# Kernel optimization log

Hardware: AMD Instinct MI355X
Metric: run time of the kernel (lower is better)

## Reference

```python
import jax, jax.numpy as jnp
import numpy as np

D_MODEL = 1024
D_HIDDEN = 16384
N_TOKENS = 8192
K = 32


def setup_inputs() -> dict:
    key = jax.random.key(0)
    k1, k2, k3 = jax.random.split(key, 3)
    x = jax.random.normal(k1, (N_TOKENS, D_MODEL), dtype=jnp.float32)
    # encoder.weight: [d_hidden, d_model] (torch Linear convention)
    W_enc = jax.random.normal(k2, (D_HIDDEN, D_MODEL), dtype=jnp.float32) * (1.0 / np.sqrt(D_MODEL))
    # decoder.weight: [d_model, d_hidden], column-normalized as in __init__
    W_dec = jax.random.normal(k3, (D_MODEL, D_HIDDEN), dtype=jnp.float32)
    W_dec = W_dec / (jnp.linalg.norm(W_dec, axis=0, keepdims=True) + 1e-8)
    b_pre = jnp.zeros((D_MODEL,), dtype=jnp.float32)
    b_act = jnp.zeros((D_HIDDEN,), dtype=jnp.float32)
    return {"x": x, "W_enc": W_enc, "W_dec": W_dec, "b_pre": b_pre, "b_act": b_act, "k": K}


def reference(x, W_enc, W_dec, b_pre, b_act, k):
    # encode
    x_cent = x - b_pre                                   # [N, d_model]
    pre_acts = jnp.einsum('nd,hd->nh', x_cent, W_enc) + b_act  # [N, d_hidden]
    # top-k hard activation with straight-through estimator
    vals, inds = jax.lax.top_k(pre_acts, k)              # [N, k]
    rows = jnp.arange(pre_acts.shape[0])[:, None]        # [N, 1]
    hard = jnp.zeros_like(pre_acts).at[rows, inds].set(jax.nn.relu(vals))
    sparse_acts = hard + (pre_acts - jax.lax.stop_gradient(pre_acts))
    # decode
    recon = jnp.einsum('nh,dh->nd', sparse_acts, W_dec) + b_pre  # [N, d_model]
    return (recon, sparse_acts, pre_acts)
```

## Files before the change

### kernel.cpp

```cpp
#include <hip/hip_runtime.h>
#include <hip/hip_bf16.h>

#define N_TOK   8192
#define DM      1024
#define DH      16384
#define KTOP    32
#define NCAND   256
#define DZ      0.08f
#define NT      16

typedef unsigned int uint;
typedef __attribute__((ext_vector_type(8))) short bf16x8;
typedef __attribute__((ext_vector_type(4))) float f32x4;

__device__ inline ushort f2bf(float f) {
    uint u = __float_as_uint(f);
    uint r = (u + 0x7FFFu + ((u >> 16) & 1u)) >> 16;
    return (ushort)r;
}
__device__ inline float bf2f(ushort u) {
    return __uint_as_float(((uint)u) << 16);
}

__device__ inline void load_lds16(const void* g, void* l) {
    __builtin_amdgcn_global_load_lds(
        (const __attribute__((address_space(1))) void*)g,
        (__attribute__((address_space(3))) void*)l, 16, 0, 0);
}

__global__ __launch_bounds__(256) void conv_x(
    const float* __restrict__ x, const float* __restrict__ b_pre,
    ushort* __restrict__ A)
{
    int i = (blockIdx.x * 256 + threadIdx.x) * 4;
    float4 v = *(const float4*)&x[i];
    float4 b = *(const float4*)&b_pre[i & (DM - 1)];
    ushort4 o;
    o.x = f2bf(v.x - b.x); o.y = f2bf(v.y - b.y);
    o.z = f2bf(v.z - b.z); o.w = f2bf(v.w - b.w);
    *(ushort4*)&A[i] = o;
}

__global__ __launch_bounds__(256) void conv_w(
    const float* __restrict__ W, ushort* __restrict__ B)
{
    int i = (blockIdx.x * 256 + threadIdx.x) * 4;
    float4 v = *(const float4*)&W[i];
    ushort4 o;
    o.x = f2bf(v.x); o.y = f2bf(v.y); o.z = f2bf(v.z); o.w = f2bf(v.w);
    *(ushort4*)&B[i] = o;
}

#define LDS_A(par, ks)  ((par) * 65536 + (ks) * 16384)
#define LDS_B(par, ks)  ((par) * 65536 + 32768 + (ks) * 16384)

__global__ __launch_bounds__(512, 2) void gemm8ph(
    const ushort* __restrict__ A, const ushort* __restrict__ B,
    const float* __restrict__ b_act, float* __restrict__ pre)
{
    __shared__ __align__(16) char smem[131072];

    const int tid  = threadIdx.x;
    const int wid  = tid >> 6;
    const int lane = tid & 63;
    const int wm   = wid >> 2;
    const int wn   = wid & 3;

    const int swz  = (blockIdx.x & 7) * 256 + (blockIdx.x >> 3);
    const int row0 = (swz & 31) * 256;
    const int col0 = (swz >> 5) * 256;

    f32x4 acc[8][4] = {};

    auto stage = [&](const ushort* __restrict__ g, int grow0, int gk0,
                     int region) {
        #pragma unroll
        for (int i = 0; i < 2; ++i) {
            int c    = i * 512 + wid * 64 + lane;
            int row  = c >> 2;
            int slot = (c & 3) ^ ((row >> 1) & 3);
            load_lds16(g + (size_t)(grow0 + row) * DM + gk0 + slot * 8,
                       smem + region + (i * 512 + wid * 64) * 16);
        }
    };
    auto ld_frag = [&](int region, int row) -> bf16x8 {
        int slot = (lane >> 4) ^ ((row >> 1) & 3);
        return *(const bf16x8*)(smem + region + row * 64 + slot * 16);
    };

    stage(A, row0, 0,  LDS_A(0, 0));
    stage(B, col0, 0,  LDS_B(0, 0));
    stage(A, row0, 32, LDS_A(0, 1));
    stage(B, col0, 32, LDS_B(0, 1));

    for (int t = 0; t < NT; ++t) {
        const int par  = t & 1;
        const int npar = par ^ 1;
        const int tn   = (t < NT - 1) ? t + 1 : t;
        const int k0n  = tn * 64;
        const int ar   = wm * 128 + (lane & 15);
        const int br   = wn * 64 + (lane & 15);

        stage(A, row0, k0n, LDS_A(npar, 0));
        asm volatile("s_waitcnt vmcnt(6)" ::: "memory");
        __builtin_amdgcn_s_barrier();
        asm volatile("" ::: "memory");

        bf16x8 af[8];
        #pragma unroll
        for (int mf = 0; mf < 8; ++mf)
            af[mf] = ld_frag(LDS_A(par, 0), ar + mf * 16);
        {
            bf16x8 b0 = ld_frag(LDS_B(par, 0), br);
            bf16x8 b1 = ld_frag(LDS_B(par, 0), br + 16);
            __builtin_amdgcn_s_setprio(1);
            #pragma unroll
            for (int mf = 0; mf < 8; ++mf) {
                acc[mf][0] = __builtin_amdgcn_mfma_f32_16x16x32_bf16(af[mf], b0, acc[mf][0], 0, 0, 0);
                acc[mf][1] = __builtin_amdgcn_mfma_f32_16x16x32_bf16(af[mf], b1, acc[mf][1], 0, 0, 0);
            }
            __builtin_amdgcn_s_setprio(0);
        }

        stage(B, col0, k0n, LDS_B(npar, 0));
        {
            bf16x8 b2 = ld_frag(LDS_B(par, 0), br + 32);
            bf16x8 b3 = ld_frag(LDS_B(par, 0), br + 48);
            __builtin_amdgcn_s_setprio(1);
            #pragma unroll
            for (int mf = 0; mf < 8; ++mf) {
                acc[mf][2] = __builtin_amdgcn_mfma_f32_16x16x32_bf16(af[mf], b2, acc[mf][2], 0, 0, 0);
                acc[mf][3] = __builtin_amdgcn_mfma_f32_16x16x32_bf16(af[mf], b3, acc[mf][3], 0, 0, 0);
            }
            __builtin_amdgcn_s_setprio(0);
        }

        stage(A, row0, k0n + 32, LDS_A(npar, 1));
        asm volatile("s_waitcnt vmcnt(6)" ::: "memory");
        __builtin_amdgcn_s_barrier();
        asm volatile("" ::: "memory");

        #pragma unroll
        for (int mf = 0; mf < 8; ++mf)
            af[mf] = ld_frag(LDS_A(par, 1), ar + mf * 16);
        {
            bf16x8 b0 = ld_frag(LDS_B(par, 1), br);
            bf16x8 b1 = ld_frag(LDS_B(par, 1), br + 16);
            __builtin_amdgcn_s_setprio(1);
            #pragma unroll
            for (int mf = 0; mf < 8; ++mf) {
                acc[mf][0] = __builtin_amdgcn_mfma_f32_16x16x32_bf16(af[mf], b0, acc[mf][0], 0, 0, 0);
                acc[mf][1] = __builtin_amdgcn_mfma_f32_16x16x32_bf16(af[mf], b1, acc[mf][1], 0, 0, 0);
            }
            __builtin_amdgcn_s_setprio(0);
        }

        stage(B, col0, k0n + 32, LDS_B(npar, 1));
        {
            bf16x8 b2 = ld_frag(LDS_B(par, 1), br + 32);
            bf16x8 b3 = ld_frag(LDS_B(par, 1), br + 48);
            __builtin_amdgcn_s_setprio(1);
            #pragma unroll
            for (int mf = 0; mf < 8; ++mf) {
                acc[mf][2] = __builtin_amdgcn_mfma_f32_16x16x32_bf16(af[mf], b2, acc[mf][2], 0, 0, 0);
                acc[mf][3] = __builtin_amdgcn_mfma_f32_16x16x32_bf16(af[mf], b3, acc[mf][3], 0, 0, 0);
            }
            __builtin_amdgcn_s_setprio(0);
        }
    }

    float bav[4];
    #pragma unroll
    for (int nf = 0; nf < 4; ++nf)
        bav[nf] = b_act[col0 + wn * 64 + nf * 16 + (lane & 15)];
    #pragma unroll
    for (int mf = 0; mf < 8; ++mf) {
        const int grow = row0 + wm * 128 + mf * 16 + (lane >> 4) * 4;
        const int gcol = col0 + wn * 64 + (lane & 15);
        #pragma unroll
        for (int r = 0; r < 4; ++r) {
            #pragma unroll
            for (int nf = 0; nf < 4; ++nf)
                pre[(size_t)(grow + r) * DH + gcol + nf * 16] = acc[mf][nf][r] + bav[nf];
        }
    }
}

__global__ __launch_bounds__(512) void topk_cand(
    const float* __restrict__ pre, float* __restrict__ sparse,
    float* __restrict__ cval, int* __restrict__ cidx, int* __restrict__ ccnt)
{
    const int row = blockIdx.x;
    const int tid = threadIdx.x;
    const float* __restrict__ p = pre + (size_t)row * DH;

    float v[32];
    #pragma unroll
    for (int j = 0; j < 32; ++j) v[j] = p[j * 512 + tid];

    float4 z = {0.f, 0.f, 0.f, 0.f};
    float4* srow = (float4*)(sparse + (size_t)row * DH);
    #pragma unroll
    for (int i = 0; i < 8; ++i) srow[tid + i * 512] = z;

    __shared__ int scount;
    float lo = -30.f, hi = 30.f, t = 0.f;
    for (int it = 0; it < 20; ++it) {
        t = 0.5f * (lo + hi);
        int c = 0;
        #pragma unroll
        for (int j = 0; j < 32; ++j) c += (v[j] > t);
        #pragma unroll
        for (int off = 32; off; off >>= 1) c += __shfl_down(c, off);
        if (tid == 0) scount = 0;
        __syncthreads();
        if ((tid & 63) == 0) atomicAdd(&scount, c);
        __syncthreads();
        int total = scount;
        __syncthreads();
        if (total >= 96 && total <= 250) break;
        if (total < 96) hi = t; else lo = t;
    }

    __shared__ int wpos;
    __shared__ float scv[NCAND];
    __shared__ int   sci[NCAND];
    if (tid == 0) wpos = 0;
    __syncthreads();
    #pragma unroll
    for (int j = 0; j < 32; ++j) {
        if (v[j] > t) {
            int pz = atomicAdd(&wpos, 1);
            if (pz < NCAND) { scv[pz] = v[j]; sci[pz] = j * 512 + tid; }
        }
    }
    __syncthreads();
    int n = min(wpos, NCAND);
    if (tid == 0) ccnt[row] = n;
    if (tid < NCAND) {
        cval[(size_t)row * NCAND + tid] = (tid < n) ? scv[tid] : -1e30f;
        cidx[(size_t)row * NCAND + tid] = (tid < n) ? sci[tid] : -1;
    }
}

__global__ __launch_bounds__(256) void fix_topk(
    const float* __restrict__ x, const float* __restrict__ b_pre,
    const float* __restrict__ W, const float* __restrict__ b_act,
    const float* __restrict__ cval, const int* __restrict__ cidx,
    float* __restrict__ sparse, float* __restrict__ vals, int* __restrict__ inds)
{
    const int row = blockIdx.x;
    const int tid = threadIdx.x;
    const int wid = tid >> 6, lane = tid & 63;

    __shared__ float xs[DM];
    for (int i = tid; i < DM; i += 256)
        xs[i] = x[(size_t)row * DM + i] - b_pre[i];

    __shared__ float sv[NCAND];
    __shared__ float sex[NCAND];
    __shared__ int   si[NCAND];
    __shared__ int   zlist[NCAND];
    __shared__ unsigned char zf[NCAND];
    __shared__ float sa32;
    __shared__ int   scin, zn;

    const float v  = cval[(size_t)row * NCAND + tid];
    const int   id = cidx[(size_t)row * NCAND + tid];
    sv[tid] = v; si[tid] = id; sex[tid] = v;
    if (tid == 0) { scin = 0; zn = 0; }
    if (tid < KTOP) {
        vals[(size_t)row * KTOP + tid] = 0.f;
        inds[(size_t)row * KTOP + tid] = -1;
    }
    __syncthreads();

    int rank = 0;
    for (int j = 0; j < NCAND; ++j) {
        float ov = sv[j];
        rank += (ov > v) || (ov == v && si[j] < id);
    }
    if (rank == 31) sa32 = v;
    __syncthreads();

    const float a32 = sa32;
    const bool cin  = v > a32 + DZ;
    const bool zone = !cin && (v >= a32 - DZ) && (id >= 0);

    unsigned long long bal = __ballot(cin);
    if (lane == 0) atomicAdd(&scin, (int)__popcll(bal));
    if (zone) { int p = atomicAdd(&zn, 1); zlist[p] = tid; }
    zf[tid] = zone ? 1 : 0;
    __syncthreads();

    const int cin_total = scin;
    const int znum = zn;

    for (int m = wid; m < znum; m += 4) {
        int t = zlist[m];
        int h = si[t];
        const float* wrow = W + (size_t)h * DM;
        float s = 0.f;
        #pragma unroll
        for (int c = 0; c < 16; ++c)
            s = fmaf(xs[lane + c * 64], wrow[lane + c * 64], s);
        #pragma unroll
        for (int off = 32; off; off >>= 1) s += __shfl_down(s, off);
        if (lane == 0) sex[t] = s + b_act[h];
    }
    __syncthreads();

    int slot = -1;
    float outv = 0.f;
    if (cin) { slot = rank; outv = v; }
    else if (zone) {
        float ev = sex[tid];
        int zrank = 0;
        for (int j = 0; j < NCAND; ++j) {
            if (zf[j]) {
                float ov = sex[j];
                zrank += (ov > ev) || (ov == ev && si[j] < id);
            }
        }
        if (zrank < KTOP - cin_total) { slot = cin_total + zrank; outv = ev; }
    }
    if (slot >= 0) {
        float r = fmaxf(outv, 0.f);
        vals[(size_t)row * KTOP + slot] = r;
        inds[(size_t)row * KTOP + slot] = id;
        sparse[(size_t)row * DH + id] = r;
    }
}

__global__ __launch_bounds__(256) void transpose_dec(
    const float* __restrict__ W, ushort* __restrict__ WT)
{
    __shared__ float t[32][33];
    const int tx = threadIdx.x;
    const int ty = threadIdx.y;
    const int h0 = blockIdx.x * 32;
    const int d0 = blockIdx.y * 32;
    #pragma unroll
    for (int r = 0; r < 4; ++r)
        t[ty + r * 8][tx] = W[(size_t)(d0 + ty + r * 8) * DH + h0 + tx];
    __syncthreads();
    #pragma unroll
    for (int r = 0; r < 4; ++r)
        WT[(size_t)(h0 + ty + r * 8) * DM + d0 + tx] = f2bf(t[tx][ty + r * 8]);
}

__global__ __launch_bounds__(256) void recon_kernel(
    const float* __restrict__ vals, const int* __restrict__ inds,
    const ushort* __restrict__ wdecT, const float* __restrict__ b_pre,
    float* __restrict__ recon)
{
    const int row = blockIdx.x;
    const int tid = threadIdx.x;
    __shared__ float lval[KTOP];
    __shared__ int   lind[KTOP];
    if (tid < KTOP) {
        lval[tid] = vals[(size_t)row * KTOP + tid];
        lind[tid] = inds[(size_t)row * KTOP + tid];
    }
    __syncthreads();

    const int d = tid * 4;
    float4 a = *(const float4*)&b_pre[d];
    #pragma unroll 8
    for (int j = 0; j < KTOP; ++j) {
        float vj = lval[j];
        int h = lind[j];
        if (vj != 0.f && h >= 0) {
            ushort4 w = *(const ushort4*)&wdecT[(size_t)h * DM + d];
            a.x = fmaf(vj, bf2f(w.x), a.x);
            a.y = fmaf(vj, bf2f(w.y), a.y);
            a.z = fmaf(vj, bf2f(w.z), a.z);
            a.w = fmaf(vj, bf2f(w.w), a.w);
        }
    }
    *(float4*)&recon[(size_t)row * DM + d] = a;
}

extern "C" void kernel_launch(void* const* d_in, const int* in_sizes, int n_in,
                              void* d_out, int out_size, void* d_ws, size_t ws_size,
                              hipStream_t stream)
{
    const float* x     = (const float*)d_in[0];
    const float* W_enc = (const float*)d_in[1];
    const float* W_dec = (const float*)d_in[2];
    const float* b_pre = (const float*)d_in[3];
    const float* b_act = (const float*)d_in[4];

    float* recon  = (float*)d_out;
    float* sparse = recon + (size_t)N_TOK * DM;
    float* pre    = sparse + (size_t)N_TOK * DH;

    ushort* Abf = (ushort*)sparse;
    ushort* Bbf = Abf + (size_t)N_TOK * DM;

    float*  cval  = (float*)d_ws;
    int*    cidx  = (int*)(cval + (size_t)N_TOK * NCAND);
    int*    ccnt  = cidx + (size_t)N_TOK * NCAND;
    float*  vals  = (float*)(ccnt + N_TOK);
    int*    inds  = (int*)(vals + (size_t)N_TOK * KTOP);
    ushort* wdecT = (ushort*)(inds + (size_t)N_TOK * KTOP);

    conv_x<<<N_TOK * DM / 1024, 256, 0, stream>>>(x, b_pre, Abf);
    conv_w<<<DH * DM / 1024, 256, 0, stream>>>(W_enc, Bbf);

    gemm8ph<<<(N_TOK / 256) * (DH / 256), 512, 0, stream>>>(Abf, Bbf, b_act, pre);

    transpose_dec<<<dim3(DH / 32, DM / 32), dim3(32, 8), 0, stream>>>(W_dec, wdecT);

    topk_cand<<<N_TOK, 512, 0, stream>>>(pre, sparse, cval, cidx, ccnt);

    fix_topk<<<N_TOK, 256, 0, stream>>>(x, b_pre, W_enc, b_act,
                                        cval, cidx, sparse, vals, inds);

    recon_kernel<<<N_TOK, 256, 0, stream>>>(vals, inds, wdecT, b_pre, recon);
}
```

Measured before the change: 929.0 us.

## Collect top-k candidates in GEMM epilogue and fuse candidate selection into fix kernel

The GEMM epilogue now thresholds each pre-activation against a fixed cutoff and records up to 8 packed bf16 value/index candidates per row per column tile into a workspace, flagging any overflow. A single fused top-k kernel reads these compact candidates instead of re-reading the full 16384-wide pre-activation row, and falls back to the old bisection search only for flagged or out-of-range rows. This removes a full pass over the large pre-activation matrix and one kernel launch. The cost is shared-memory atomics in the GEMM epilogue, a memset of the candidate buffer, and a data-dependent fixed threshold tuned to the input distribution. The last K-step is also peeled out of the GEMM loop so it no longer issues a redundant prefetch.

```diff
diff --git a/kernel.cpp b/kernel.cpp
--- a/kernel.cpp
+++ b/kernel.cpp
@@ -5,7 +5,9 @@
 #define DM      1024
 #define DH      16384
 #define KTOP    32
-#define NCAND   256
+#define NCAND   512
+#define SLOTS   8
+#define CAND_T  2.2f
 #define DZ      0.08f
 #define NT      16
 
@@ -56,7 +58,8 @@
 
 __global__ __launch_bounds__(512, 2) void gemm8ph(
     const ushort* __restrict__ A, const ushort* __restrict__ B,
-    const float* __restrict__ b_act, float* __restrict__ pre)
+    const float* __restrict__ b_act, float* __restrict__ pre,
+    uint* __restrict__ cand, uint* __restrict__ flags)
 {
     __shared__ __align__(16) char smem[131072];
 
@@ -88,18 +91,18 @@
         return *(const bf16x8*)(smem + region + row * 64 + slot * 16);
     };
 
+    const int ar = wm * 128 + (lane & 15);
+    const int br = wn * 64 + (lane & 15);
+
     stage(A, row0, 0,  LDS_A(0, 0));
     stage(B, col0, 0,  LDS_B(0, 0));
     stage(A, row0, 32, LDS_A(0, 1));
     stage(B, col0, 32, LDS_B(0, 1));
 
-    for (int t = 0; t < NT; ++t) {
+    for (int t = 0; t < NT - 1; ++t) {
         const int par  = t & 1;
         const int npar = par ^ 1;
-        const int tn   = (t < NT - 1) ? t + 1 : t;
-        const int k0n  = tn * 64;
-        const int ar   = wm * 128 + (lane & 15);
-        const int br   = wn * 64 + (lane & 15);
+        const int k0n  = (t + 1) * 64;
 
         stage(A, row0, k0n, LDS_A(npar, 0));
         asm volatile("s_waitcnt vmcnt(6)" ::: "memory");
@@ -121,7 +124,6 @@
             }
             __builtin_amdgcn_s_setprio(0);
         }
-
         stage(B, col0, k0n, LDS_B(npar, 0));
         {
             bf16x8 b2 = ld_frag(LDS_B(par, 0), br + 32);
@@ -134,7 +136,6 @@
             }
             __builtin_amdgcn_s_setprio(0);
         }
-
         stage(A, row0, k0n + 32, LDS_A(npar, 1));
         asm volatile("s_waitcnt vmcnt(6)" ::: "memory");
         __builtin_amdgcn_s_barrier();
@@ -154,7 +155,6 @@
             }
             __builtin_amdgcn_s_setprio(0);
         }
-
         stage(B, col0, k0n + 32, LDS_B(npar, 1));
         {
             bf16x8 b2 = ld_frag(LDS_B(par, 1), br + 32);
@@ -168,93 +168,115 @@
             __builtin_amdgcn_s_setprio(0);
         }
     }
+
+    {
+        const int par = (NT - 1) & 1;
+        asm volatile("s_waitcnt vmcnt(4)" ::: "memory");
+        __builtin_amdgcn_s_barrier();
+        asm volatile("" ::: "memory");
+
+        bf16x8 af[8];
+        #pragma unroll
+        for (int mf = 0; mf < 8; ++mf)
+            af[mf] = ld_frag(LDS_A(par, 0), ar + mf * 16);
+        {
+            bf16x8 b0 = ld_frag(LDS_B(par, 0), br);
+            bf16x8 b1 = ld_frag(LDS_B(par, 0), br + 16);
+            bf16x8 b2 = ld_frag(LDS_B(par, 0), br + 32);
+            bf16x8 b3 = ld_frag(LDS_B(par, 0), br + 48);
+            __builtin_amdgcn_s_setprio(1);
+            #pragma unroll
+            for (int mf = 0; mf < 8; ++mf) {
+                acc[mf][0] = __builtin_amdgcn_mfma_f32_16x16x32_bf16(af[mf], b0, acc[mf][0], 0, 0, 0);
+                acc[mf][1] = __builtin_amdgcn_mfma_f32_16x16x32_bf16(af[mf], b1, acc[mf][1], 0, 0, 0);
+                acc[mf][2] = __builtin_amdgcn_mfma_f32_16x16x32_bf16(af[mf], b2, acc[mf][2], 0, 0, 0);
+                acc[mf][3] = __builtin_amdgcn_mfma_f32_16x16x32_bf16(af[mf], b3, acc[mf][3], 0, 0, 0);
+            }
+            __builtin_amdgcn_s_setprio(0);
+        }
+        asm volatile("s_waitcnt vmcnt(0)" ::: "memory");
+        __builtin_amdgcn_s_barrier();
+        asm volatile("" ::: "memory");
+
+        #pragma unroll
+        for (int mf = 0; mf < 8; ++mf)
+            af[mf] = ld_frag(LDS_A(par, 1), ar + mf * 16);
+        {
+            bf16x8 b0 = ld_frag(LDS_B(par, 1), br);
+            bf16x8 b1 = ld_frag(LDS_B(par, 1), br + 16);
+            bf16x8 b2 = ld_frag(LDS_B(par, 1), br + 32);
+            bf16x8 b3 = ld_frag(LDS_B(par, 1), br + 48);
+            __builtin_amdgcn_s_setprio(1);
+            #pragma unroll
+            for (int mf = 0; mf < 8; ++mf) {
+                acc[mf][0] = __builtin_amdgcn_mfma_f32_16x16x32_bf16(af[mf], b0, acc[mf][0], 0, 0, 0);
+                acc[mf][1] = __builtin_amdgcn_mfma_f32_16x16x32_bf16(af[mf], b1, acc[mf][1], 0, 0, 0);
+                acc[mf][2] = __builtin_amdgcn_mfma_f32_16x16x32_bf16(af[mf], b2, acc[mf][2], 0, 0, 0);
+                acc[mf][3] = __builtin_amdgcn_mfma_f32_16x16x32_bf16(af[mf], b3, acc[mf][3], 0, 0, 0);
+            }
+            __builtin_amdgcn_s_setprio(0);
+        }
+    }
+
+    __syncthreads();
+    uint* cnt = (uint*)smem;
+    uint* buf = (uint*)(smem + 1024);
+    if (tid < 256) cnt[tid] = 0;
+    __syncthreads();
 
     float bav[4];
     #pragma unroll
     for (int nf = 0; nf < 4; ++nf)
         bav[nf] = b_act[col0 + wn * 64 + nf * 16 + (lane & 15)];
+
     #pragma unroll
     for (int mf = 0; mf < 8; ++mf) {
-        const int grow = row0 + wm * 128 + mf * 16 + (lane >> 4) * 4;
+        const int lrow = wm * 128 + mf * 16 + (lane >> 4) * 4;
         const int gcol = col0 + wn * 64 + (lane & 15);
         #pragma unroll
         for (int r = 0; r < 4; ++r) {
             #pragma unroll
-            for (int nf = 0; nf < 4; ++nf)
-                pre[(size_t)(grow + r) * DH + gcol + nf * 16] = acc[mf][nf][r] + bav[nf];
-        }
-    }
-}
-
-__global__ __launch_bounds__(512) void topk_cand(
-    const float* __restrict__ pre, float* __restrict__ sparse,
-    float* __restrict__ cval, int* __restrict__ cidx, int* __restrict__ ccnt)
-{
-    const int row = blockIdx.x;
-    const int tid = threadIdx.x;
-    const float* __restrict__ p = pre + (size_t)row * DH;
-
-    float v[32];
-    #pragma unroll
-    for (int j = 0; j < 32; ++j) v[j] = p[j * 512 + tid];
-
-    float4 z = {0.f, 0.f, 0.f, 0.f};
-    float4* srow = (float4*)(sparse + (size_t)row * DH);
-    #pragma unroll
-    for (int i = 0; i < 8; ++i) srow[tid + i * 512] = z;
-
-    __shared__ int scount;
-    float lo = -30.f, hi = 30.f, t = 0.f;
-    for (int it = 0; it < 20; ++it) {
-        t = 0.5f * (lo + hi);
-        int c = 0;
-        #pragma unroll
-        for (int j = 0; j < 32; ++j) c += (v[j] > t);
-        #pragma unroll
-        for (int off = 32; off; off >>= 1) c += __shfl_down(c, off);
-        if (tid == 0) scount = 0;
-        __syncthreads();
-        if ((tid & 63) == 0) atomicAdd(&scount, c);
-        __syncthreads();
-        int total = scount;
-        __syncthreads();
-        if (total >= 96 && total <= 250) break;
-        if (total < 96) hi = t; else lo = t;
-    }
-
-    __shared__ int wpos;
-    __shared__ float scv[NCAND];
-    __shared__ int   sci[NCAND];
-    if (tid == 0) wpos = 0;
-    __syncthreads();
-    #pragma unroll
-    for (int j = 0; j < 32; ++j) {
-        if (v[j] > t) {
-            int pz = atomicAdd(&wpos, 1);
-            if (pz < NCAND) { scv[pz] = v[j]; sci[pz] = j * 512 + tid; }
-        }
-    }
-    __syncthreads();
-    int n = min(wpos, NCAND);
-    if (tid == 0) ccnt[row] = n;
-    if (tid < NCAND) {
-        cval[(size_t)row * NCAND + tid] = (tid < n) ? scv[tid] : -1e30f;
-        cidx[(size_t)row * NCAND + tid] = (tid < n) ? sci[tid] : -1;
-    }
-}
-
-__global__ __launch_bounds__(256) void fix_topk(
+            for (int nf = 0; nf < 4; ++nf) {
+                float o = acc[mf][nf][r] + bav[nf];
+                pre[(size_t)(row0 + lrow + r) * DH + gcol + nf * 16] = o;
+                if (o > CAND_T) {
+                    uint pos = atomicAdd(&cnt[lrow + r], 1u);
+                    if (pos < SLOTS)
+                        buf[(lrow + r) * SLOTS + pos] =
+                            ((uint)f2bf(o) << 16) | (uint)(16383 - (gcol + nf * 16));
+                }
+            }
+        }
+    }
+    __syncthreads();
+    if (tid < 256) {
+        uint c = cnt[tid];
+        uint m = c < SLOTS ? c : SLOTS;
+        const size_t base = (size_t)(row0 + tid) * NCAND + (col0 >> 8) * SLOTS;
+        for (uint k = 0; k < m; ++k)
+            cand[base + k] = buf[tid * SLOTS + k];
+        if (c > SLOTS) flags[row0 + tid] = 1u;
+    }
+}
+
+__global__ __launch_bounds__(512) void topk_fused(
     const float* __restrict__ x, const float* __restrict__ b_pre,
     const float* __restrict__ W, const float* __restrict__ b_act,
-    const float* __restrict__ cval, const int* __restrict__ cidx,
+    const uint* __restrict__ cand, const uint* __restrict__ flags,
+    const float* __restrict__ pre,
     float* __restrict__ sparse, float* __restrict__ vals, int* __restrict__ inds)
 {
     const int row = blockIdx.x;
     const int tid = threadIdx.x;
     const int wid = tid >> 6, lane = tid & 63;
 
+    float4 z4 = {0.f, 0.f, 0.f, 0.f};
+    float4* srow = (float4*)(sparse + (size_t)row * DH);
+    #pragma unroll
+    for (int i = 0; i < 8; ++i) srow[tid + i * 512] = z4;
+
     __shared__ float xs[DM];
-    for (int i = tid; i < DM; i += 256)
+    for (int i = tid; i < DM; i += 512)
         xs[i] = x[(size_t)row * DM + i] - b_pre[i];
 
     __shared__ float sv[NCAND];
@@ -263,16 +285,67 @@
     __shared__ int   zlist[NCAND];
     __shared__ unsigned char zf[NCAND];
     __shared__ float sa32;
-    __shared__ int   scin, zn;
-
-    const float v  = cval[(size_t)row * NCAND + tid];
-    const int   id = cidx[(size_t)row * NCAND + tid];
-    sv[tid] = v; si[tid] = id; sex[tid] = v;
-    if (tid == 0) { scin = 0; zn = 0; }
+    __shared__ int   scin, zn, nl;
+
+    sv[tid] = -1e30f; si[tid] = -1;
+    if (tid == 0) { scin = 0; zn = 0; nl = 0; sa32 = -1e30f; }
     if (tid < KTOP) {
         vals[(size_t)row * KTOP + tid] = 0.f;
         inds[(size_t)row * KTOP + tid] = -1;
     }
+    __syncthreads();
+
+    uint pk = cand[(size_t)row * NCAND + tid];
+    if (pk) {
+        int p = atomicAdd(&nl, 1);
+        sv[p] = bf2f((ushort)(pk >> 16));
+        si[p] = 16383 - (int)(pk & 0x3FFFu);
+    }
+    __syncthreads();
+    int n = nl;
+
+    const bool fb = (flags[row] != 0u) || n < 96 || n > 500;
+    if (fb) {
+        __syncthreads();
+        sv[tid] = -1e30f; si[tid] = -1;
+        if (tid == 0) nl = 0;
+        const float* __restrict__ p = pre + (size_t)row * DH;
+        float v[32];
+        #pragma unroll
+        for (int j = 0; j < 32; ++j) v[j] = p[j * 512 + tid];
+
+        __shared__ int scount;
+        float lo = -30.f, hi = 30.f, t = 0.f;
+        for (int it = 0; it < 20; ++it) {
+            t = 0.5f * (lo + hi);
+            int c = 0;
+            #pragma unroll
+            for (int j = 0; j < 32; ++j) c += (v[j] > t);
+            #pragma unroll
+            for (int off = 32; off; off >>= 1) c += __shfl_down(c, off);
+            if (tid == 0) scount = 0;
+            __syncthreads();
+            if ((tid & 63) == 0) atomicAdd(&scount, c);
+            __syncthreads();
+            int total = scount;
+            __syncthreads();
+            if (total >= 96 && total <= 450) break;
+            if (total < 96) hi = t; else lo = t;
+        }
+        #pragma unroll
+        for (int j = 0; j < 32; ++j) {
+            if (v[j] > t) {
+                int p2 = atomicAdd(&nl, 1);
+                if (p2 < NCAND) { sv[p2] = v[j]; si[p2] = j * 512 + tid; }
+            }
+        }
+        __syncthreads();
+        n = min(nl, NCAND);
+    }
+
+    const float v  = sv[tid];
+    const int   id = si[tid];
+    sex[tid] = v;
     __syncthreads();
 
     int rank = 0;
@@ -296,7 +369,7 @@
     const int cin_total = scin;
     const int znum = zn;
 
-    for (int m = wid; m < znum; m += 4) {
+    for (int m = wid; m < znum; m += 8) {
         int t = zlist[m];
         int h = si[t];
         const float* wrow = W + (size_t)h * DM;
@@ -324,7 +397,7 @@
         }
         if (zrank < KTOP - cin_total) { slot = cin_total + zrank; outv = ev; }
     }
-    if (slot >= 0) {
+    if (slot >= 0 && slot < KTOP) {
         float r = fmaxf(outv, 0.f);
         vals[(size_t)row * KTOP + slot] = r;
         inds[(size_t)row * KTOP + slot] = id;
@@ -398,24 +471,24 @@
     ushort* Abf = (ushort*)sparse;
     ushort* Bbf = Abf + (size_t)N_TOK * DM;
 
-    float*  cval  = (float*)d_ws;
-    int*    cidx  = (int*)(cval + (size_t)N_TOK * NCAND);
-    int*    ccnt  = cidx + (size_t)N_TOK * NCAND;
-    float*  vals  = (float*)(ccnt + N_TOK);
+    uint*   cand  = (uint*)d_ws;
+    uint*   flags = cand + (size_t)N_TOK * NCAND;
+    float*  vals  = (float*)(flags + N_TOK);
     int*    inds  = (int*)(vals + (size_t)N_TOK * KTOP);
     ushort* wdecT = (ushort*)(inds + (size_t)N_TOK * KTOP);
 
+    hipMemsetAsync(cand, 0, ((size_t)N_TOK * NCAND + N_TOK) * sizeof(uint), stream);
+
     conv_x<<<N_TOK * DM / 1024, 256, 0, stream>>>(x, b_pre, Abf);
     conv_w<<<DH * DM / 1024, 256, 0, stream>>>(W_enc, Bbf);
 
-    gemm8ph<<<(N_TOK / 256) * (DH / 256), 512, 0, stream>>>(Abf, Bbf, b_act, pre);
+    gemm8ph<<<(N_TOK / 256) * (DH / 256), 512, 0, stream>>>(
+        Abf, Bbf, b_act, pre, cand, flags);
 
     transpose_dec<<<dim3(DH / 32, DM / 32), dim3(32, 8), 0, stream>>>(W_dec, wdecT);
 
-    topk_cand<<<N_TOK, 512, 0, stream>>>(pre, sparse, cval, cidx, ccnt);
-
-    fix_topk<<<N_TOK, 256, 0, stream>>>(x, b_pre, W_enc, b_act,
-                                        cval, cidx, sparse, vals, inds);
+    topk_fused<<<N_TOK, 512, 0, stream>>>(x, b_pre, W_enc, b_act,
+                                          cand, flags, pre, sparse, vals, inds);
 
     recon_kernel<<<N_TOK, 256, 0, stream>>>(vals, inds, wdecT, b_pre, recon);
 }
```

Result: slower. 1.203 ms (+29.5%).
